# Kernel optimization log

Measured on AMD Instinct MI355X. Metric: run time of the kernel, lower is better.

Reference implementation:

```python
import jax, jax.numpy as jnp
import numpy as np

N, E = 10000, 160000
F_IN, H1, C1, C2 = 256, 8, 128, 128
SLOPE = 0.2  # PyG GATConv default negative_slope


def setup_inputs() -> dict:
    key = jax.random.key(0)
    ks = jax.random.split(key, 9)
    s = 0.05
    return {
        "x": jax.random.normal(ks[0], (N, F_IN), jnp.float32),
        "edge_index": jax.random.randint(ks[1], (2, E), 0, N),
        "W1": jax.random.normal(ks[2], (F_IN, H1 * C1), jnp.float32) * s,
        "a_src1": jax.random.normal(ks[3], (H1, C1), jnp.float32) * s,
        "a_dst1": jax.random.normal(ks[4], (H1, C1), jnp.float32) * s,
        "b1": jnp.zeros((H1 * C1,), jnp.float32),
        "W2": jax.random.normal(ks[5], (H1 * C1, C2), jnp.float32) * s,
        "a_src2": jax.random.normal(ks[6], (1, C2), jnp.float32) * s,
        "a_dst2": jax.random.normal(ks[7], (1, C2), jnp.float32) * s,
        "b2": jnp.zeros((C2,), jnp.float32),
    }


def gat_conv(x, src, dst, W, a_s, a_d, b, heads, out_ch, concat):
    n = x.shape[0]
    h = (x @ W).reshape(n, heads, out_ch)            # [N,H,C]
    s_src = jnp.einsum("nhc,hc->nh", h, a_s)         # [N,H]
    s_dst = jnp.einsum("nhc,hc->nh", h, a_d)
    e = jax.nn.leaky_relu(s_src[src] + s_dst[dst], SLOPE)   # [Etot,H]
    # segment softmax over incoming edges per destination (self-loops guarantee non-empty segments)
    m = jax.lax.stop_gradient(jax.ops.segment_max(e, dst, num_segments=n))
    p = jnp.exp(e - m[dst])
    denom = jax.ops.segment_sum(p, dst, num_segments=n)
    alpha = p / denom[dst]                            # [Etot,H]
    out = jax.ops.segment_sum(h[src] * alpha[:, :, None], dst, num_segments=n)  # [N,H,C]
    out = out.reshape(n, heads * out_ch) if concat else out.mean(axis=1)
    return out + b


def reference(x, edge_index, W1, a_src1, a_dst1, b1, W2, a_src2, a_dst2, b2):
    n = x.shape[0]
    loops = jnp.arange(n, dtype=edge_index.dtype)     # PyG add_self_loops=True
    src = jnp.concatenate([edge_index[0], loops])
    dst = jnp.concatenate([edge_index[1], loops])
    # dropout layers are identity at inference (training=False)
    h1 = jax.nn.elu(gat_conv(x, src, dst, W1, a_src1, a_dst1, b1, H1, C1, True))
    return gat_conv(h1, src, dst, W2, a_src2, a_dst2, b2, 1, C2, False)
```

## Files before the change

### kernel.cpp

```cpp
#include <hip/hip_runtime.h>
#include <math.h>

#define F_IN 256
#define H1 8
#define C1 128
#define HC1 1024
#define C2 128
#define SLOPE 0.2f

typedef unsigned short u16;
typedef __attribute__((ext_vector_type(8))) short bf16x8;
typedef __attribute__((ext_vector_type(4))) float f32x4;


__device__ __forceinline__ float lrelu(float v) { return v > 0.f ? v : SLOPE * v; }

__device__ __forceinline__ unsigned bf16_rne(float x) {
    unsigned u = __float_as_uint(x);
    u += 0x7fffu + ((u >> 16) & 1u);
    return u >> 16;
}

__device__ __forceinline__ void split2(float a, float b, unsigned& hi, unsigned& lo) {
    unsigned ha = bf16_rne(a), hb = bf16_rne(b);
    float fa = __uint_as_float(ha << 16), fb = __uint_as_float(hb << 16);
    hi = ha | (hb << 16);
    lo = bf16_rne(a - fa) | (bf16_rne(b - fb) << 16);
}

__device__ __forceinline__ void gload16(const u16* g, u16* l) {
    __builtin_amdgcn_global_load_lds(
        (const __attribute__((address_space(1))) unsigned*)g,
        (__attribute__((address_space(3))) unsigned*)l, 16, 0, 0);
}


__global__ void init_deg(int* deg, int n) {
    int i = blockIdx.x * blockDim.x + threadIdx.x;
    if (i < n) deg[i] = 1;
}

__global__ void hist_kernel(const int* __restrict__ dst, int* __restrict__ deg, int E) {
    int i = blockIdx.x * blockDim.x + threadIdx.x;
    if (i < E) atomicAdd(&deg[dst[i]], 1);
}

__global__ void scan_kernel(const int* __restrict__ deg, int* __restrict__ start,
                            int* __restrict__ cursor, int n) {
    __shared__ int buf[1024];
    int carry = 0;
    for (int base = 0; base < n; base += 1024) {
        int i = base + (int)threadIdx.x;
        int v = (i < n) ? deg[i] : 0;
        buf[threadIdx.x] = v;
        __syncthreads();
        for (int offd = 1; offd < 1024; offd <<= 1) {
            int tv = 0;
            if ((int)threadIdx.x >= offd) tv = buf[threadIdx.x - offd];
            __syncthreads();
            if ((int)threadIdx.x >= offd) buf[threadIdx.x] += tv;
            __syncthreads();
        }
        int incl = buf[threadIdx.x];
        if (i < n) { start[i] = carry + incl - v; cursor[i] = carry + incl - v; }
        carry += buf[1023];
        __syncthreads();
    }
    if (threadIdx.x == 0) start[n] = carry;
}

__global__ void scatter_kernel(const int* __restrict__ src, const int* __restrict__ dst,
                               int* __restrict__ cursor, int* __restrict__ ssorted,
                               unsigned char* __restrict__ rowloc,
                               int E, int N) {
    int i = blockIdx.x * blockDim.x + threadIdx.x;
    if (i < E) {
        int d = dst[i];
        int pos = atomicAdd(&cursor[d], 1);
        ssorted[pos] = src[i];
        rowloc[pos] = (unsigned char)(d & 15);
    } else if (i < E + N) {
        int d = i - E;
        int pos = atomicAdd(&cursor[d], 1);
        ssorted[pos] = d;
        rowloc[pos] = (unsigned char)(d & 15);
    }
}


__global__ void split_mat(const float* __restrict__ in, u16* __restrict__ hi,
                          u16* __restrict__ lo, int n) {
    int i = blockIdx.x * blockDim.x + threadIdx.x;
    if (i >= n) return;
    float v = in[i];
    unsigned h = bf16_rne(v);
    hi[i] = (u16)h;
    lo[i] = (u16)bf16_rne(v - __uint_as_float(h << 16));
}

__global__ void split_transpose(const float* __restrict__ in, u16* __restrict__ hi,
                                u16* __restrict__ lo, int R, int C) {
    int i = blockIdx.x * blockDim.x + threadIdx.x;
    if (i >= R * C) return;
    int r = i / C, c = i % C;
    float v = in[i];
    unsigned h = bf16_rne(v);
    hi[(size_t)c * R + r] = (u16)h;
    lo[(size_t)c * R + r] = (u16)bf16_rne(v - __uint_as_float(h << 16));
}


__global__ __launch_bounds__(256) void gemm_mfma(const u16* __restrict__ Ahi,
                                                 const u16* __restrict__ Alo,
                                                 const u16* __restrict__ Bhi,
                                                 const u16* __restrict__ Blo,
                                                 u16* __restrict__ Cbf,
                                                 int M, int N, int K) {
    __shared__ u16 lds[16384];
    const int t = threadIdx.x;
    const int rbase = blockIdx.y * 128;
    const int cbase = blockIdx.x * 128;

    const int lane = t & 63;
    const int R0 = (t >> 7) << 6;
    const int C0 = ((t >> 6) & 1) << 6;
    const int lrow = lane & 15;
    const int kq = lane >> 4;

    f32x4 acc[4][4] = {};

    for (int k0 = 0; k0 < K; k0 += 32) {
#pragma unroll
        for (int i = 0; i < 2; i++) {
            int c = t + (i << 8);
            int row = c >> 2;
            int kc = (c & 3) << 3;
            int ar = min(rbase + row, M - 1);
            int br = cbase + row;
            gload16(Ahi + (size_t)ar * K + k0 + kc, &lds[c * 8]);
            gload16(Alo + (size_t)ar * K + k0 + kc, &lds[4096 + c * 8]);
            gload16(Bhi + (size_t)br * K + k0 + kc, &lds[8192 + c * 8]);
            gload16(Blo + (size_t)br * K + k0 + kc, &lds[12288 + c * 8]);
        }
        __syncthreads();

        bf16x8 ah[4], al[4], bh[4], bl[4];
#pragma unroll
        for (int m = 0; m < 4; m++) {
            int off = (R0 + (m << 4) + lrow) * 32 + (kq << 3);
            ah[m] = *(const bf16x8*)&lds[off];
            al[m] = *(const bf16x8*)&lds[4096 + off];
        }
#pragma unroll
        for (int n = 0; n < 4; n++) {
            int off = (C0 + (n << 4) + lrow) * 32 + (kq << 3);
            bh[n] = *(const bf16x8*)&lds[8192 + off];
            bl[n] = *(const bf16x8*)&lds[12288 + off];
        }
#pragma unroll
        for (int m = 0; m < 4; m++)
#pragma unroll
            for (int n = 0; n < 4; n++) {
                acc[m][n] = __builtin_amdgcn_mfma_f32_16x16x32_bf16(ah[m], bh[n], acc[m][n], 0, 0, 0);
                acc[m][n] = __builtin_amdgcn_mfma_f32_16x16x32_bf16(ah[m], bl[n], acc[m][n], 0, 0, 0);
                acc[m][n] = __builtin_amdgcn_mfma_f32_16x16x32_bf16(al[m], bh[n], acc[m][n], 0, 0, 0);
            }
        __syncthreads();
    }

#pragma unroll
    for (int m = 0; m < 4; m++)
#pragma unroll
        for (int n = 0; n < 4; n++) {
            int col = cbase + C0 + (n << 4) + lrow;
#pragma unroll
            for (int r = 0; r < 4; r++) {
                int row = rbase + R0 + (m << 4) + kq * 4 + r;
                if (row < M) Cbf[(size_t)row * N + col] = (u16)bf16_rne(acc[m][n][r]);
            }
        }
}


__global__ __launch_bounds__(256) void gemm_mfma64(const u16* __restrict__ Ahi,
                                                   const u16* __restrict__ Alo,
                                                   const u16* __restrict__ Bhi,
                                                   const u16* __restrict__ Blo,
                                                   u16* __restrict__ Cbf,
                                                   int M, int N, int K) {
    __shared__ u16 lds[8192];
    const int t = threadIdx.x;
    const int rbase = blockIdx.y * 64;
    const int cbase = blockIdx.x * 64;

    const int lane = t & 63;
    const int w = t >> 6;
    const int R0 = (w >> 1) << 5;
    const int C0 = (w & 1) << 5;
    const int lrow = lane & 15;
    const int kq = lane >> 4;

    f32x4 acc[2][2] = {};

    for (int k0 = 0; k0 < K; k0 += 32) {
        {
            int row = t >> 2;
            int kc = (t & 3) << 3;
            int ar = min(rbase + row, M - 1);
            int br = cbase + row;
            gload16(Ahi + (size_t)ar * K + k0 + kc, &lds[t * 8]);
            gload16(Alo + (size_t)ar * K + k0 + kc, &lds[2048 + t * 8]);
            gload16(Bhi + (size_t)br * K + k0 + kc, &lds[4096 + t * 8]);
            gload16(Blo + (size_t)br * K + k0 + kc, &lds[6144 + t * 8]);
        }
        __syncthreads();

        bf16x8 ah[2], al[2], bh[2], bl[2];
#pragma unroll
        for (int m = 0; m < 2; m++) {
            int off = (R0 + (m << 4) + lrow) * 32 + (kq << 3);
            ah[m] = *(const bf16x8*)&lds[off];
            al[m] = *(const bf16x8*)&lds[2048 + off];
        }
#pragma unroll
        for (int n = 0; n < 2; n++) {
            int off = (C0 + (n << 4) + lrow) * 32 + (kq << 3);
            bh[n] = *(const bf16x8*)&lds[4096 + off];
            bl[n] = *(const bf16x8*)&lds[6144 + off];
        }
#pragma unroll
        for (int m = 0; m < 2; m++)
#pragma unroll
            for (int n = 0; n < 2; n++) {
                acc[m][n] = __builtin_amdgcn_mfma_f32_16x16x32_bf16(ah[m], bh[n], acc[m][n], 0, 0, 0);
                acc[m][n] = __builtin_amdgcn_mfma_f32_16x16x32_bf16(ah[m], bl[n], acc[m][n], 0, 0, 0);
                acc[m][n] = __builtin_amdgcn_mfma_f32_16x16x32_bf16(al[m], bh[n], acc[m][n], 0, 0, 0);
            }
        __syncthreads();
    }

#pragma unroll
    for (int m = 0; m < 2; m++)
#pragma unroll
        for (int n = 0; n < 2; n++) {
            int col = cbase + C0 + (n << 4) + lrow;
#pragma unroll
            for (int r = 0; r < 4; r++) {
                int row = rbase + R0 + (m << 4) + kq * 4 + r;
                if (row < M) Cbf[(size_t)row * N + col] = (u16)bf16_rne(acc[m][n][r]);
            }
        }
}


__global__ __launch_bounds__(256) void scores1_bf(const unsigned* __restrict__ hbf,
                                                  const float* __restrict__ a_s,
                                                  const float* __restrict__ a_d,
                                                  float* __restrict__ ssrc,
                                                  float* __restrict__ sdst, int N) {
    int wid = blockIdx.x * 4 + (threadIdx.x >> 6);
    if (wid >= N * H1) return;
    int lane = threadIdx.x & 63;
    int n = wid >> 3, hh = wid & 7;
    unsigned u = hbf[(size_t)n * 512 + hh * 64 + lane];
    float c0 = __uint_as_float(u << 16);
    float c1 = __uint_as_float(u & 0xffff0000u);
    const float* as = a_s + hh * C1;
    const float* ad = a_d + hh * C1;
    float vs = c0 * as[2 * lane] + c1 * as[2 * lane + 1];
    float vd = c0 * ad[2 * lane] + c1 * ad[2 * lane + 1];
    for (int off = 32; off; off >>= 1) {
        vs += __shfl_xor(vs, off);
        vd += __shfl_xor(vd, off);
    }
    if (lane == 0) { ssrc[wid] = vs; sdst[wid] = vd; }
}

__global__ __launch_bounds__(256) void scores2_bf(const unsigned* __restrict__ hbf,
                                                  const float* __restrict__ a_s,
                                                  const float* __restrict__ a_d,
                                                  float* __restrict__ ssrc,
                                                  float* __restrict__ sdst, int N) {
    int n = blockIdx.x * 4 + (threadIdx.x >> 6);
    if (n >= N) return;
    int lane = threadIdx.x & 63;
    unsigned u = hbf[(size_t)n * 64 + lane];
    float c0 = __uint_as_float(u << 16);
    float c1 = __uint_as_float(u & 0xffff0000u);
    float vs = c0 * a_s[2 * lane] + c1 * a_s[2 * lane + 1];
    float vd = c0 * a_d[2 * lane] + c1 * a_d[2 * lane + 1];
    for (int off = 32; off; off >>= 1) {
        vs += __shfl_xor(vs, off);
        vd += __shfl_xor(vd, off);
    }
    if (lane == 0) { ssrc[n] = vs; sdst[n] = vd; }
}


__global__ __launch_bounds__(256) void softmax_edges1(
    const float* __restrict__ ssrc, const float* __restrict__ sdst,
    const int* __restrict__ start, const int* __restrict__ ssorted,
    float* __restrict__ alphab, int N, int ET) {
    int lane = threadIdx.x & 63;
    int p = lane & 15, g = lane >> 4;
    int task = (blockIdx.x * 4 + (threadIdx.x >> 6)) * 4 + g;
    if (task >= N * H1) return;
    int d = task >> 3, hh = task & 7;
    int s0 = start[d], ne = start[d + 1] - s0;
    float sd = sdst[d * H1 + hh];
    int src0 = 0; float v0 = -1e30f;
    if (p < ne) { src0 = ssorted[s0 + p]; v0 = lrelu(ssrc[src0 * H1 + hh] + sd); }
    float m = v0;
    for (int e = p + 16; e < ne; e += 16)
        m = fmaxf(m, lrelu(ssrc[ssorted[s0 + e] * H1 + hh] + sd));
    for (int o = 8; o; o >>= 1) m = fmaxf(m, __shfl_xor(m, o));
    float p0 = (p < ne) ? __expf(v0 - m) : 0.f;
    float s = p0;
    for (int e = p + 16; e < ne; e += 16)
        s += __expf(lrelu(ssrc[ssorted[s0 + e] * H1 + hh] + sd) - m);
    for (int o = 8; o; o >>= 1) s += __shfl_xor(s, o);
    float inv = 1.f / s;
    float* ab = alphab + (size_t)hh * ET;
    if (p < ne) ab[s0 + p] = p0 * inv;
    for (int e = p + 16; e < ne; e += 16)
        ab[s0 + e] = __expf(lrelu(ssrc[ssorted[s0 + e] * H1 + hh] + sd) - m) * inv;
}


__global__ __launch_bounds__(256) void agg_mfma1(
    const u16* __restrict__ hbf,
    const float* __restrict__ alphab,
    const unsigned char* __restrict__ rowloc,
    const int* __restrict__ start,
    const int* __restrict__ ssorted,
    const float* __restrict__ bias,
    u16* __restrict__ outHi, u16* __restrict__ outLo,
    int N, int ET) {
    __shared__ unsigned A32[2][16 * 68];
    __shared__ int mOff[2][64];

    const int hh = blockIdx.x & 7;
    const int g = blockIdx.x >> 3;
    const int t = threadIdx.x;
    const int w = t >> 6;
    const int lane = t & 63;
    const int cl = lane & 15, q = lane >> 4;

    const int d0 = g * 16;
    const int e0 = start[d0], e1 = start[min(d0 + 16, N)];
    const float* ab = alphab + (size_t)hh * ET;

    const int lanebyte = hh * 256 + w * 64 + 4 * cl;
    const char* hbase = (const char*)hbf;

    const int nk = (e1 - e0 + 63) >> 6;

    auto fill = [&](int b, int kb) {
        unsigned* Az = &A32[b][(lane >> 2) * 68 + (lane & 3) * 16];
        uint4 z = {0u, 0u, 0u, 0u};
        *(uint4*)(Az) = z;
        *(uint4*)(Az + 4) = z;
        *(uint4*)(Az + 8) = z;
        *(uint4*)(Az + 12) = z;
        int pos = kb + lane;
        bool valid = pos < e1;
        int ps = valid ? pos : e0;
        float af = valid ? ab[ps] : 0.f;
        unsigned ahiu = bf16_rne(af);
        unsigned alou = bf16_rne(af - __uint_as_float(ahiu << 16));
        int rr = rowloc[ps];
        mOff[b][lane] = ssorted[ps] << 11;
        asm volatile("s_waitcnt lgkmcnt(0)" ::: "memory");
        A32[b][rr * 68 + lane] = ahiu | (alou << 16);
    };

    f32x4 acc0 = {}, acc1 = {};

    if (w == 0 && nk > 0) fill(0, e0);

    for (int i = 0; i < nk; ++i) {
        __syncthreads();
        const int b = i & 1;
        if (w == 0 && i + 1 < nk) fill(b ^ 1, e0 + (i + 1) * 64);

        const int mb = q * 8;
        int4 o0 = *(const int4*)&mOff[b][mb];
        int4 o1 = *(const int4*)&mOff[b][mb + 4];
        int4 o2 = *(const int4*)&mOff[b][32 + mb];
        int4 o3 = *(const int4*)&mOff[b][32 + mb + 4];
        int oo[16] = {o0.x, o0.y, o0.z, o0.w, o1.x, o1.y, o1.z, o1.w,
                      o2.x, o2.y, o2.z, o2.w, o3.x, o3.y, o3.z, o3.w};

        unsigned gld[16];
#pragma unroll
        for (int j = 0; j < 16; j++)
            gld[j] = *(const unsigned*)(hbase + (unsigned)(oo[j] + lanebyte));

        const unsigned* Ar = &A32[b][cl * 68 + mb];
        uint4 a0 = *(const uint4*)(Ar);
        uint4 a1 = *(const uint4*)(Ar + 4);
        uint4 a2 = *(const uint4*)(Ar + 32);
        uint4 a3 = *(const uint4*)(Ar + 36);
        unsigned aw[16] = {a0.x, a0.y, a0.z, a0.w, a1.x, a1.y, a1.z, a1.w,
                           a2.x, a2.y, a2.z, a2.w, a3.x, a3.y, a3.z, a3.w};

        union { unsigned u[4]; bf16x8 v; } ahi0, alo0, ahi1, alo1, b00, b10, b01, b11;
#pragma unroll
        for (int r = 0; r < 4; r++) {
            ahi0.u[r] = __builtin_amdgcn_perm(aw[2 * r + 1], aw[2 * r], 0x05040100u);
            alo0.u[r] = __builtin_amdgcn_perm(aw[2 * r + 1], aw[2 * r], 0x07060302u);
            ahi1.u[r] = __builtin_amdgcn_perm(aw[8 + 2 * r + 1], aw[8 + 2 * r], 0x05040100u);
            alo1.u[r] = __builtin_amdgcn_perm(aw[8 + 2 * r + 1], aw[8 + 2 * r], 0x07060302u);
            b00.u[r] = __builtin_amdgcn_perm(gld[2 * r + 1], gld[2 * r], 0x05040100u);
            b10.u[r] = __builtin_amdgcn_perm(gld[2 * r + 1], gld[2 * r], 0x07060302u);
            b01.u[r] = __builtin_amdgcn_perm(gld[8 + 2 * r + 1], gld[8 + 2 * r], 0x05040100u);
            b11.u[r] = __builtin_amdgcn_perm(gld[8 + 2 * r + 1], gld[8 + 2 * r], 0x07060302u);
        }

        acc0 = __builtin_amdgcn_mfma_f32_16x16x32_bf16(ahi0.v, b00.v, acc0, 0, 0, 0);
        acc0 = __builtin_amdgcn_mfma_f32_16x16x32_bf16(alo0.v, b00.v, acc0, 0, 0, 0);
        acc1 = __builtin_amdgcn_mfma_f32_16x16x32_bf16(ahi0.v, b10.v, acc1, 0, 0, 0);
        acc1 = __builtin_amdgcn_mfma_f32_16x16x32_bf16(alo0.v, b10.v, acc1, 0, 0, 0);
        acc0 = __builtin_amdgcn_mfma_f32_16x16x32_bf16(ahi1.v, b01.v, acc0, 0, 0, 0);
        acc0 = __builtin_amdgcn_mfma_f32_16x16x32_bf16(alo1.v, b01.v, acc0, 0, 0, 0);
        acc1 = __builtin_amdgcn_mfma_f32_16x16x32_bf16(ahi1.v, b11.v, acc1, 0, 0, 0);
        acc1 = __builtin_amdgcn_mfma_f32_16x16x32_bf16(alo1.v, b11.v, acc1, 0, 0, 0);
    }

    {
        int chbase = w * 32 + 2 * cl;
        float bv0 = bias[hh * C1 + chbase];
        float bv1 = bias[hh * C1 + chbase + 1];
#pragma unroll
        for (int r = 0; r < 4; r++) {
            int d = d0 + q * 4 + r;
            if (d >= N) continue;
            float v0 = acc0[r] + bv0;
            float v1 = acc1[r] + bv1;
            v0 = v0 > 0.f ? v0 : expm1f(v0);
            v1 = v1 > 0.f ? v1 : expm1f(v1);
            unsigned hi, lo;
            split2(v0, v1, hi, lo);
            size_t idx = (size_t)d * HC1 + hh * C1 + chbase;
            ((unsigned*)outHi)[idx >> 1] = hi;
            ((unsigned*)outLo)[idx >> 1] = lo;
        }
    }
}


template<int H, bool SPLITOUT>
__global__ __launch_bounds__(256) void agg_bf(const unsigned* __restrict__ hbf,
                                              const float* __restrict__ ssrc,
                                              const float* __restrict__ sdst,
                                              const int* __restrict__ start,
                                              const int* __restrict__ ssorted,
                                              const float* __restrict__ bias,
                                              float* __restrict__ out,
                                              unsigned* __restrict__ outHi,
                                              unsigned* __restrict__ outLo, int N) {
    int hh, grp;
    if (H == 8) { hh = blockIdx.x & 7; grp = blockIdx.x >> 3; }
    else        { hh = 0;              grp = blockIdx.x; }
    int wid = threadIdx.x >> 6, lane = threadIdx.x & 63;
    int d = grp * 4 + wid;
    if (d >= N) return;
    const int g = lane >> 4, p = lane & 15;
    int s0 = start[d];
    int ne = start[d + 1] - s0;
    float sd = sdst[d * H + hh];

    const unsigned* hlane = hbf + hh * 64 + p * 4;
    const int rowstride = H * 64;

    int src0 = 0; float v0 = -1e30f;
    if (lane < ne) { src0 = ssorted[s0 + lane]; v0 = lrelu(ssrc[src0 * H + hh] + sd); }
    float m = v0;
    for (int e = lane + 64; e < ne; e += 64)
        m = fmaxf(m, lrelu(ssrc[ssorted[s0 + e] * H + hh] + sd));
    for (int o = 32; o; o >>= 1) m = fmaxf(m, __shfl_xor(m, o));

    float p0 = (lane < ne) ? __expf(v0 - m) : 0.f;
    float ssum = p0;
    for (int e = lane + 64; e < ne; e += 64)
        ssum += __expf(lrelu(ssrc[ssorted[s0 + e] * H + hh] + sd) - m);
    for (int o = 32; o; o >>= 1) ssum += __shfl_xor(ssum, o);
    float inv = 1.f / ssum;

    float acc[8] = {};
    for (int base = 0; base < ne; base += 64) {
        int srcr; float al;
        if (base == 0) { srcr = src0; al = p0 * inv; }
        else {
            srcr = 0; al = 0.f;
            int e = base + lane;
            if (e < ne) {
                srcr = ssorted[s0 + e];
                al = __expf(lrelu(ssrc[srcr * H + hh] + sd) - m) * inv;
            }
        }
        int cnt = min(64, ne - base);
        for (int e2 = 0; e2 < cnt; e2 += 4) {
            float a = __shfl(al, e2 + g);
            int sr = __shfl(srcr, e2 + g);
            uint4 u = *(const uint4*)(hlane + (size_t)sr * rowstride);
            acc[0] += a * __uint_as_float(u.x << 16);
            acc[1] += a * __uint_as_float(u.x & 0xffff0000u);
            acc[2] += a * __uint_as_float(u.y << 16);
            acc[3] += a * __uint_as_float(u.y & 0xffff0000u);
            acc[4] += a * __uint_as_float(u.z << 16);
            acc[5] += a * __uint_as_float(u.z & 0xffff0000u);
            acc[6] += a * __uint_as_float(u.w << 16);
            acc[7] += a * __uint_as_float(u.w & 0xffff0000u);
        }
    }

#pragma unroll
    for (int i = 0; i < 8; i++) {
        acc[i] += __shfl_xor(acc[i], 16);
        acc[i] += __shfl_xor(acc[i], 32);
    }

    float r0 = g == 0 ? acc[0] : g == 1 ? acc[2] : g == 2 ? acc[4] : acc[6];
    float r1 = g == 0 ? acc[1] : g == 1 ? acc[3] : g == 2 ? acc[5] : acc[7];
    int j = 4 * p + g;
    float2 bv = ((const float2*)bias)[hh * 64 + j];
    r0 += bv.x; r1 += bv.y;
    size_t idx = (size_t)d * (H * 64) + hh * 64 + j;
    if (SPLITOUT) {
        r0 = r0 > 0.f ? r0 : expm1f(r0);
        r1 = r1 > 0.f ? r1 : expm1f(r1);
        unsigned hi, lo;
        split2(r0, r1, hi, lo);
        outHi[idx] = hi;
        outLo[idx] = lo;
    } else {
        ((float2*)out)[idx] = make_float2(r0, r1);
    }
}


extern "C" void kernel_launch(void* const* d_in, const int* in_sizes, int n_in,
                              void* d_out, int out_size, void* d_ws, size_t ws_size,
                              hipStream_t stream) {
    const float* x      = (const float*)d_in[0];
    const int*   ei     = (const int*)d_in[1];
    const float* W1     = (const float*)d_in[2];
    const float* a_src1 = (const float*)d_in[3];
    const float* a_dst1 = (const float*)d_in[4];
    const float* b1     = (const float*)d_in[5];
    const float* W2     = (const float*)d_in[6];
    const float* a_src2 = (const float*)d_in[7];
    const float* a_dst2 = (const float*)d_in[8];
    const float* b2     = (const float*)d_in[9];
    float* out = (float*)d_out;

    int E = in_sizes[1] / 2;
    int N = in_sizes[0] / F_IN;
    int ET = E + N;
    const int* esrc = ei;
    const int* edst = ei + E;

    char* ws = (char*)d_ws;
    size_t off = 0;
    auto alloc = [&](size_t bytes) -> char* {
        char* p = ws + off;
        off = (off + bytes + 255) & ~(size_t)255;
        return p;
    };
    u16* x_hi    = (u16*)alloc((size_t)N * F_IN * 2);
    u16* x_lo    = (u16*)alloc((size_t)N * F_IN * 2);
    u16* W1t_hi  = (u16*)alloc((size_t)F_IN * HC1 * 2);
    u16* W1t_lo  = (u16*)alloc((size_t)F_IN * HC1 * 2);
    u16* W2t_hi  = (u16*)alloc((size_t)HC1 * C2 * 2);
    u16* W2t_lo  = (u16*)alloc((size_t)HC1 * C2 * 2);
    u16* h1_bf   = (u16*)alloc((size_t)N * HC1 * 2);
    u16* h1a_hi  = (u16*)alloc((size_t)N * HC1 * 2);
    u16* h1a_lo  = (u16*)alloc((size_t)N * HC1 * 2);
    u16* h2_bf   = (u16*)alloc((size_t)N * C2 * 2);
    float* ss1   = (float*)alloc((size_t)N * H1 * 4);
    float* sd1   = (float*)alloc((size_t)N * H1 * 4);
    float* ss2   = (float*)alloc((size_t)N * 4);
    float* sd2   = (float*)alloc((size_t)N * 4);
    int* deg     = (int*)alloc((size_t)N * 4);
    int* startp  = (int*)alloc((size_t)(N + 1) * 4);
    int* cursor  = (int*)alloc((size_t)N * 4);
    int* ssorted = (int*)alloc((size_t)ET * 4);
    unsigned char* rowloc = (unsigned char*)alloc((size_t)ET);
    float* alpha1 = (float*)x_hi;

    init_deg<<<(N + 255) / 256, 256, 0, stream>>>(deg, N);
    hist_kernel<<<(E + 255) / 256, 256, 0, stream>>>(edst, deg, E);
    scan_kernel<<<1, 1024, 0, stream>>>(deg, startp, cursor, N);
    scatter_kernel<<<(E + N + 255) / 256, 256, 0, stream>>>(esrc, edst, cursor, ssorted, rowloc, E, N);

    split_mat<<<(N * F_IN + 255) / 256, 256, 0, stream>>>(x, x_hi, x_lo, N * F_IN);
    split_transpose<<<(F_IN * HC1 + 255) / 256, 256, 0, stream>>>(W1, W1t_hi, W1t_lo, F_IN, HC1);
    split_transpose<<<(HC1 * C2 + 255) / 256, 256, 0, stream>>>(W2, W2t_hi, W2t_lo, HC1, C2);

    gemm_mfma<<<dim3(HC1 / 128, (N + 127) / 128), 256, 0, stream>>>(
        x_hi, x_lo, W1t_hi, W1t_lo, h1_bf, N, HC1, F_IN);
    scores1_bf<<<(N * H1 + 3) / 4, 256, 0, stream>>>(
        (const unsigned*)h1_bf, a_src1, a_dst1, ss1, sd1, N);
    softmax_edges1<<<(N * H1 + 15) / 16, 256, 0, stream>>>(
        ss1, sd1, startp, ssorted, alpha1, N, ET);
    agg_mfma1<<<((N + 15) / 16) * H1, 256, 0, stream>>>(
        h1_bf, alpha1, rowloc, startp, ssorted, b1, h1a_hi, h1a_lo, N, ET);

    gemm_mfma64<<<dim3(C2 / 64, (N + 63) / 64), 256, 0, stream>>>(
        h1a_hi, h1a_lo, W2t_hi, W2t_lo, h2_bf, N, C2, HC1);
    scores2_bf<<<(N + 3) / 4, 256, 0, stream>>>(
        (const unsigned*)h2_bf, a_src2, a_dst2, ss2, sd2, N);
    agg_bf<1, false><<<(N + 3) / 4, 256, 0, stream>>>(
        (const unsigned*)h2_bf, ss2, sd2, startp, ssorted, b2,
        out, nullptr, nullptr, N);
}
```

Measured before the change: 250.7 us.

## Fuse edge softmax into layer-1 aggregation and double K-step in gemm_mfma64

Removes the separate softmax_edges1 kernel: each agg_mfma1 block now computes the per-destination max and inverse sum for its 16 destinations into shared memory, then recomputes each edge's attention weight on the fly while filling the MFMA operand tile. This drops the alpha write and read through global memory and one launch. In exchange the max/sum work is repeated once per head block and the fill path gains an exp. Separately, gemm_mfma64 now loads 64 K-elements per stage into a doubled LDS buffer, halving the number of barrier pairs per tile.

```diff
diff --git a/kernel.cpp b/kernel.cpp
--- a/kernel.cpp
+++ b/kernel.cpp
@@ -188,7 +188,7 @@
                                                    const u16* __restrict__ Blo,
                                                    u16* __restrict__ Cbf,
                                                    int M, int N, int K) {
-    __shared__ u16 lds[8192];
+    __shared__ u16 lds[16384];
     const int t = threadIdx.x;
     const int rbase = blockIdx.y * 64;
     const int cbase = blockIdx.x * 64;
@@ -202,40 +202,49 @@
 
     f32x4 acc[2][2] = {};
 
-    for (int k0 = 0; k0 < K; k0 += 32) {
+    for (int k0 = 0; k0 < K; k0 += 64) {
         {
-            int row = t >> 2;
-            int kc = (t & 3) << 3;
+            int row = (w << 4) + (lane >> 2);
+            int kcc = (lane & 3) << 3;
             int ar = min(rbase + row, M - 1);
             int br = cbase + row;
-            gload16(Ahi + (size_t)ar * K + k0 + kc, &lds[t * 8]);
-            gload16(Alo + (size_t)ar * K + k0 + kc, &lds[2048 + t * 8]);
-            gload16(Bhi + (size_t)br * K + k0 + kc, &lds[4096 + t * 8]);
-            gload16(Blo + (size_t)br * K + k0 + kc, &lds[6144 + t * 8]);
+            const size_t ga = (size_t)ar * K + k0 + kcc;
+            const size_t gb = (size_t)br * K + k0 + kcc;
+            const int ldo = row * 32 + kcc;
+#pragma unroll
+            for (int s2 = 0; s2 < 2; s2++) {
+                gload16(Ahi + ga + s2 * 32, &lds[s2 * 2048 + ldo]);
+                gload16(Alo + ga + s2 * 32, &lds[4096 + s2 * 2048 + ldo]);
+                gload16(Bhi + gb + s2 * 32, &lds[8192 + s2 * 2048 + ldo]);
+                gload16(Blo + gb + s2 * 32, &lds[12288 + s2 * 2048 + ldo]);
+            }
         }
         __syncthreads();
 
-        bf16x8 ah[2], al[2], bh[2], bl[2];
-#pragma unroll
-        for (int m = 0; m < 2; m++) {
-            int off = (R0 + (m << 4) + lrow) * 32 + (kq << 3);
-            ah[m] = *(const bf16x8*)&lds[off];
-            al[m] = *(const bf16x8*)&lds[2048 + off];
-        }
-#pragma unroll
-        for (int n = 0; n < 2; n++) {
-            int off = (C0 + (n << 4) + lrow) * 32 + (kq << 3);
-            bh[n] = *(const bf16x8*)&lds[4096 + off];
-            bl[n] = *(const bf16x8*)&lds[6144 + off];
-        }
-#pragma unroll
-        for (int m = 0; m < 2; m++)
+#pragma unroll
+        for (int s = 0; s < 2; s++) {
+            bf16x8 ah[2], al[2], bh[2], bl[2];
+#pragma unroll
+            for (int m = 0; m < 2; m++) {
+                int off = s * 2048 + (R0 + (m << 4) + lrow) * 32 + (kq << 3);
+                ah[m] = *(const bf16x8*)&lds[off];
+                al[m] = *(const bf16x8*)&lds[4096 + off];
+            }
 #pragma unroll
             for (int n = 0; n < 2; n++) {
-                acc[m][n] = __builtin_amdgcn_mfma_f32_16x16x32_bf16(ah[m], bh[n], acc[m][n], 0, 0, 0);
-                acc[m][n] = __builtin_amdgcn_mfma_f32_16x16x32_bf16(ah[m], bl[n], acc[m][n], 0, 0, 0);
-                acc[m][n] = __builtin_amdgcn_mfma_f32_16x16x32_bf16(al[m], bh[n], acc[m][n], 0, 0, 0);
+                int off = s * 2048 + (C0 + (n << 4) + lrow) * 32 + (kq << 3);
+                bh[n] = *(const bf16x8*)&lds[8192 + off];
+                bl[n] = *(const bf16x8*)&lds[12288 + off];
             }
+#pragma unroll
+            for (int m = 0; m < 2; m++)
+#pragma unroll
+                for (int n = 0; n < 2; n++) {
+                    acc[m][n] = __builtin_amdgcn_mfma_f32_16x16x32_bf16(ah[m], bh[n], acc[m][n], 0, 0, 0);
+                    acc[m][n] = __builtin_amdgcn_mfma_f32_16x16x32_bf16(ah[m], bl[n], acc[m][n], 0, 0, 0);
+                    acc[m][n] = __builtin_amdgcn_mfma_f32_16x16x32_bf16(al[m], bh[n], acc[m][n], 0, 0, 0);
+                }
+        }
         __syncthreads();
     }
 
@@ -297,47 +306,19 @@
 }
 
 
-__global__ __launch_bounds__(256) void softmax_edges1(
-    const float* __restrict__ ssrc, const float* __restrict__ sdst,
-    const int* __restrict__ start, const int* __restrict__ ssorted,
-    float* __restrict__ alphab, int N, int ET) {
-    int lane = threadIdx.x & 63;
-    int p = lane & 15, g = lane >> 4;
-    int task = (blockIdx.x * 4 + (threadIdx.x >> 6)) * 4 + g;
-    if (task >= N * H1) return;
-    int d = task >> 3, hh = task & 7;
-    int s0 = start[d], ne = start[d + 1] - s0;
-    float sd = sdst[d * H1 + hh];
-    int src0 = 0; float v0 = -1e30f;
-    if (p < ne) { src0 = ssorted[s0 + p]; v0 = lrelu(ssrc[src0 * H1 + hh] + sd); }
-    float m = v0;
-    for (int e = p + 16; e < ne; e += 16)
-        m = fmaxf(m, lrelu(ssrc[ssorted[s0 + e] * H1 + hh] + sd));
-    for (int o = 8; o; o >>= 1) m = fmaxf(m, __shfl_xor(m, o));
-    float p0 = (p < ne) ? __expf(v0 - m) : 0.f;
-    float s = p0;
-    for (int e = p + 16; e < ne; e += 16)
-        s += __expf(lrelu(ssrc[ssorted[s0 + e] * H1 + hh] + sd) - m);
-    for (int o = 8; o; o >>= 1) s += __shfl_xor(s, o);
-    float inv = 1.f / s;
-    float* ab = alphab + (size_t)hh * ET;
-    if (p < ne) ab[s0 + p] = p0 * inv;
-    for (int e = p + 16; e < ne; e += 16)
-        ab[s0 + e] = __expf(lrelu(ssrc[ssorted[s0 + e] * H1 + hh] + sd) - m) * inv;
-}
-
-
 __global__ __launch_bounds__(256) void agg_mfma1(
     const u16* __restrict__ hbf,
-    const float* __restrict__ alphab,
+    const float* __restrict__ ssrc,
+    const float* __restrict__ sdst,
     const unsigned char* __restrict__ rowloc,
     const int* __restrict__ start,
     const int* __restrict__ ssorted,
     const float* __restrict__ bias,
     u16* __restrict__ outHi, u16* __restrict__ outLo,
-    int N, int ET) {
+    int N) {
     __shared__ unsigned A32[2][16 * 68];
     __shared__ int mOff[2][64];
+    __shared__ float sM[16], sInv[16], sDl[16];
 
     const int hh = blockIdx.x & 7;
     const int g = blockIdx.x >> 3;
@@ -348,7 +329,26 @@
 
     const int d0 = g * 16;
     const int e0 = start[d0], e1 = start[min(d0 + 16, N)];
-    const float* ab = alphab + (size_t)hh * ET;
+
+    {
+        int j = t >> 4;
+        int p2 = t & 15;
+        int dj = d0 + j;
+        if (dj < N) {
+            int s0 = start[dj], ne = start[dj + 1] - s0;
+            float sd = sdst[dj * H1 + hh];
+            float mloc = -1e30f;
+            for (int e = p2; e < ne; e += 16)
+                mloc = fmaxf(mloc, lrelu(ssrc[ssorted[s0 + e] * H1 + hh] + sd));
+            for (int o = 8; o; o >>= 1) mloc = fmaxf(mloc, __shfl_xor(mloc, o));
+            float sloc = 0.f;
+            for (int e = p2; e < ne; e += 16)
+                sloc += __expf(lrelu(ssrc[ssorted[s0 + e] * H1 + hh] + sd) - mloc);
+            for (int o = 8; o; o >>= 1) sloc += __shfl_xor(sloc, o);
+            if (p2 == 0) { sM[j] = mloc; sInv[j] = 1.f / sloc; sDl[j] = sd; }
+        }
+    }
+    __syncthreads();
 
     const int lanebyte = hh * 256 + w * 64 + 4 * cl;
     const char* hbase = (const char*)hbf;
@@ -365,11 +365,14 @@
         int pos = kb + lane;
         bool valid = pos < e1;
         int ps = valid ? pos : e0;
-        float af = valid ? ab[ps] : 0.f;
+        int src = ssorted[ps];
+        int rr = rowloc[ps];
+        float af = valid
+            ? __expf(lrelu(ssrc[src * H1 + hh] + sDl[rr]) - sM[rr]) * sInv[rr]
+            : 0.f;
         unsigned ahiu = bf16_rne(af);
         unsigned alou = bf16_rne(af - __uint_as_float(ahiu << 16));
-        int rr = rowloc[ps];
-        mOff[b][lane] = ssorted[ps] << 11;
+        mOff[b][lane] = src << 11;
         asm volatile("s_waitcnt lgkmcnt(0)" ::: "memory");
         A32[b][rr * 68 + lane] = ahiu | (alou << 16);
     };
@@ -587,7 +590,6 @@
     int* cursor  = (int*)alloc((size_t)N * 4);
     int* ssorted = (int*)alloc((size_t)ET * 4);
     unsigned char* rowloc = (unsigned char*)alloc((size_t)ET);
-    float* alpha1 = (float*)x_hi;
 
     init_deg<<<(N + 255) / 256, 256, 0, stream>>>(deg, N);
     hist_kernel<<<(E + 255) / 256, 256, 0, stream>>>(edst, deg, E);
@@ -602,10 +604,8 @@
         x_hi, x_lo, W1t_hi, W1t_lo, h1_bf, N, HC1, F_IN);
     scores1_bf<<<(N * H1 + 3) / 4, 256, 0, stream>>>(
         (const unsigned*)h1_bf, a_src1, a_dst1, ss1, sd1, N);
-    softmax_edges1<<<(N * H1 + 15) / 16, 256, 0, stream>>>(
-        ss1, sd1, startp, ssorted, alpha1, N, ET);
     agg_mfma1<<<((N + 15) / 16) * H1, 256, 0, stream>>>(
-        h1_bf, alpha1, rowloc, startp, ssorted, b1, h1a_hi, h1a_lo, N, ET);
+        h1_bf, ss1, sd1, rowloc, startp, ssorted, b1, h1a_hi, h1a_lo, N);
 
     gemm_mfma64<<<dim3(C2 / 64, (N + 63) / 64), 256, 0, stream>>>(
         h1a_hi, h1a_lo, W2t_hi, W2t_lo, h2_bf, N, C2, HC1);
```

New measurement: 251.5 us. No clear change (+0.3%).
